# Kernel optimization log

Measured on AMD Instinct MI355X. Metric: run time of the kernel, lower is better.

The kernel has to match this reference:

```python
import jax, jax.numpy as jnp
import numpy as np

E = 32          # n_routed_experts
H = 2048        # hidden_size
I = 1024        # moe_intermediate_size
T = 32768       # total routed tokens (grouped/sorted by expert)


def setup_inputs() -> dict:
    key = jax.random.key(0)
    k1, k2, k3 = jax.random.split(key, 3)
    x = jax.random.normal(k1, (T, H), dtype=jnp.float32)
    # per-expert weights: fused w1/w3 -> [E, H, 2I], w2 -> [E, I, H]
    w13 = jax.random.normal(k2, (E, H, 2 * I), dtype=jnp.float32) * (1.0 / np.sqrt(H))
    w2 = jax.random.normal(k3, (E, I, H), dtype=jnp.float32) * (1.0 / np.sqrt(I))
    tokens_per_expert = jnp.full((E,), T // E, dtype=jnp.int32)  # uniform groups
    decoding = 0  # unused flag (prefill path)
    return {"x": x, "w13": w13, "w2": w2,
            "tokens_per_expert": tokens_per_expert, "decoding": decoding}


def reference(x, w13, w2, tokens_per_expert, decoding):
    # Grouped GEMM expert FFN with SwiGLU. Tokens are grouped (sorted) by
    # expert; with uniform tokens_per_expert the ragged grouped GEMM is the
    # block-diagonal einsum below (g = tokens per expert group).
    e = w13.shape[0]
    t = x.shape[0]
    g = t // e
    xg = x.reshape(e, g, x.shape[-1])            # [E, g, H]
    gate_up = jnp.einsum('egi,eio->ego', xg, w13)  # [E, g, 2I]
    gate, up = jnp.split(gate_up, 2, axis=-1)
    h = jax.nn.silu(gate) * up                    # fused SwiGLU epilogue
    out = jnp.einsum('egi,eio->ego', h, w2)       # [E, g, H]
    return out.reshape(t, -1)
```

## Files before the change

kernel.cpp:

```cpp
#include <hip/hip_runtime.h>
#include <hip/hip_bf16.h>

#define NE 32
#define HD 2048
#define ID 1024
#define GT 1024

#define BK 64

typedef __attribute__((ext_vector_type(8))) __bf16 bf16x8;
typedef __attribute__((ext_vector_type(4))) float  f32x4;

__device__ __forceinline__ __bf16 f2b(float f) { return (__bf16)f; }

__device__ __forceinline__ bf16x8 pack8(const f32x4 a, const f32x4 b) {
  bf16x8 v;
  v[0] = f2b(a[0]); v[1] = f2b(a[1]); v[2] = f2b(a[2]); v[3] = f2b(a[3]);
  v[4] = f2b(b[0]); v[5] = f2b(b[1]); v[6] = f2b(b[2]); v[7] = f2b(b[3]);
  return v;
}

__global__ __launch_bounds__(256)
void cvt_x_bf16(const float* __restrict__ x, __bf16* __restrict__ xb) {
  size_t i = ((size_t)blockIdx.x * 256 + threadIdx.x) * 8;
  f32x4 a = *reinterpret_cast<const f32x4*>(x + i);
  f32x4 b = *reinterpret_cast<const f32x4*>(x + i + 4);
  *reinterpret_cast<bf16x8*>(xb + i) = pack8(a, b);
}

__global__ __launch_bounds__(512, 2)
void moe_gemm1_swiglu_bA(const __bf16* __restrict__ xb,
                         const float* __restrict__ w13,
                         __bf16* __restrict__ h) {
  __shared__ __bf16 As[2][256][BK];
  __shared__ __bf16 Bg[2][128][BK];
  __shared__ __bf16 Bu[2][128][BK];

  const int t = threadIdx.x;
  const int bid  = blockIdx.x;
  const int work = (bid & 7) * 128 + (bid >> 3);
  const int e    = work >> 5;
  const int rem  = work & 31;
  const int n0   = (rem >> 2) * 128;
  const int m0   = (rem & 3) * 256;

  const __bf16* xA = xb + (size_t)(e * GT + m0) * HD;
  const float*  wB = w13 + (size_t)e * HD * (2 * ID);

  const int wid = t >> 6, lane = t & 63;
  const int wm = wid >> 2, wn = wid & 3;
  const int fr = lane & 15, fq = lane >> 4;

  const int tb = t & 255;
  const int nq = tb & 31;
  const int ko = tb >> 5;
  const int bcol = (t < 256 ? 0 : ID) + n0 + nq * 4;
  __bf16 (*Bm)[128][BK] = (t < 256) ? Bg : Bu;

  f32x4 accg[8][2];
  f32x4 accu[8][2];
#pragma unroll
  for (int i = 0; i < 8; ++i)
#pragma unroll
    for (int j = 0; j < 2; ++j) { accg[i][j] = 0.f; accu[i][j] = 0.f; }

  bf16x8 raa[4];
  f32x4 rb[8];

#define LOAD_TILE1(K0)                                                         \
  do {                                                                         \
    _Pragma("unroll")                                                          \
    for (int i = 0; i < 4; ++i) {                                              \
      int id = i * 512 + t;                                                    \
      int koA = id & 7, m = id >> 3;                                           \
      raa[i] = *reinterpret_cast<const bf16x8*>(xA + (size_t)m * HD + (K0) + koA * 8); \
    }                                                                          \
    const float* pb = wB + (size_t)((K0) + ko * 8) * (2 * ID) + bcol;          \
    _Pragma("unroll")                                                          \
    for (int j = 0; j < 8; ++j)                                                \
      rb[j] = *reinterpret_cast<const f32x4*>(pb + (size_t)j * (2 * ID));      \
  } while (0)

#define STORE_TILE1(P)                                                         \
  do {                                                                         \
    _Pragma("unroll")                                                          \
    for (int i = 0; i < 4; ++i) {                                              \
      int id = i * 512 + t;                                                    \
      int koA = id & 7, m = id >> 3;                                           \
      *reinterpret_cast<bf16x8*>(&As[P][m][(koA ^ (m & 7)) * 8]) = raa[i];     \
    }                                                                          \
    _Pragma("unroll")                                                          \
    for (int c = 0; c < 4; ++c) {                                              \
      int row = nq * 4 + c;                                                    \
      int slot = (ko ^ ((row >> 1) & 7)) * 8;                                  \
      bf16x8 v;                                                                \
      _Pragma("unroll")                                                        \
      for (int j = 0; j < 8; ++j) v[j] = f2b(rb[j][c]);                        \
      *reinterpret_cast<bf16x8*>(&Bm[P][row][slot]) = v;                       \
    }                                                                          \
  } while (0)

#define MFMA_HALF1(P, KB)                                                      \
  do {                                                                         \
    bf16x8 af[8], bgf[2], buf2[2];                                             \
    _Pragma("unroll")                                                          \
    for (int mi = 0; mi < 8; ++mi) {                                           \
      int row = wm * 128 + mi * 16 + fr;                                       \
      int oct = (fq + (KB)) ^ (row & 7);                                       \
      af[mi] = *reinterpret_cast<const bf16x8*>(&As[P][row][oct * 8]);         \
    }                                                                          \
    _Pragma("unroll")                                                          \
    for (int ni = 0; ni < 2; ++ni) {                                           \
      int row = wn * 32 + ni * 16 + fr;                                        \
      int oct = (fq + (KB)) ^ ((row >> 1) & 7);                                \
      bgf[ni]  = *reinterpret_cast<const bf16x8*>(&Bg[P][row][oct * 8]);       \
      buf2[ni] = *reinterpret_cast<const bf16x8*>(&Bu[P][row][oct * 8]);       \
    }                                                                          \
    __builtin_amdgcn_s_setprio(1);                                             \
    _Pragma("unroll")                                                          \
    for (int mi = 0; mi < 8; ++mi)                                             \
      _Pragma("unroll")                                                        \
      for (int ni = 0; ni < 2; ++ni) {                                         \
        accg[mi][ni] = __builtin_amdgcn_mfma_f32_16x16x32_bf16(                \
            af[mi], bgf[ni], accg[mi][ni], 0, 0, 0);                           \
        accu[mi][ni] = __builtin_amdgcn_mfma_f32_16x16x32_bf16(                \
            af[mi], buf2[ni], accu[mi][ni], 0, 0, 0);                          \
      }                                                                        \
    __builtin_amdgcn_s_setprio(0);                                             \
  } while (0)

  LOAD_TILE1(0);
  STORE_TILE1(0);
  LOAD_TILE1(BK);
  asm volatile("s_waitcnt lgkmcnt(0)" ::: "memory");
  __builtin_amdgcn_s_barrier();

  for (int k0 = 0, p = 0; k0 < HD; k0 += BK, p ^= 1) {
    MFMA_HALF1(p, 0);
    if (k0 + BK < HD) STORE_TILE1(p ^ 1);
    MFMA_HALF1(p, 4);
    if (k0 + 2 * BK < HD) LOAD_TILE1(k0 + 2 * BK);
    asm volatile("s_waitcnt lgkmcnt(0)" ::: "memory");
    __builtin_amdgcn_s_barrier();
  }
#undef LOAD_TILE1
#undef STORE_TILE1
#undef MFMA_HALF1

#pragma unroll
  for (int mi = 0; mi < 8; ++mi)
#pragma unroll
    for (int ni = 0; ni < 2; ++ni)
#pragma unroll
      for (int j = 0; j < 4; ++j) {
        int row = m0 + wm * 128 + mi * 16 + fq * 4 + j;
        int col = n0 + wn * 32 + ni * 16 + fr;
        float g = accg[mi][ni][j];
        float u = accu[mi][ni][j];
        float s = g / (1.f + __expf(-g));
        h[(size_t)(e * GT + row) * ID + col] = f2b(s * u);
      }
}

__global__ __launch_bounds__(256, 2)
void moe_gemm1_swiglu(const float* __restrict__ x,
                      const float* __restrict__ w13,
                      __bf16* __restrict__ h) {
  __shared__ __bf16 As[2][128][BK];
  __shared__ __bf16 Bg[2][64][BK];
  __shared__ __bf16 Bu[2][64][BK];

  const int t  = threadIdx.x;
  const int e  = blockIdx.z;
  const int m0 = blockIdx.y * 128;
  const int n0 = blockIdx.x * 64;

  const float* xA = x   + (size_t)(e * GT + m0) * HD;
  const float* wB = w13 + (size_t)e * HD * (2 * ID);

  const int wid = t >> 6, lane = t & 63;
  const int wm = wid >> 1, wn = wid & 1;
  const int fr = lane & 15, fq = lane >> 4;

  const int tb = t & 127;
  const int nq = tb & 15;
  const int ko = tb >> 4;
  const int bcol = (t < 128 ? 0 : ID) + n0 + nq * 4;
  __bf16 (*Bm)[64][BK] = (t < 128) ? Bg : Bu;

  f32x4 accg[4][2];
  f32x4 accu[4][2];
#pragma unroll
  for (int i = 0; i < 4; ++i)
#pragma unroll
    for (int j = 0; j < 2; ++j) { accg[i][j] = 0.f; accu[i][j] = 0.f; }

  f32x4 ra[4][2];
  f32x4 rb[8];

#define LOAD_TILE1(K0)                                                         \
  do {                                                                         \
    _Pragma("unroll")                                                          \
    for (int i = 0; i < 4; ++i) {                                              \
      int id = i * 256 + t;                                                    \
      int r = id >> 3, oc = id & 7;                                            \
      const float* src = xA + (size_t)r * HD + (K0) + oc * 8;                  \
      ra[i][0] = *reinterpret_cast<const f32x4*>(src);                         \
      ra[i][1] = *reinterpret_cast<const f32x4*>(src + 4);                     \
    }                                                                          \
    const float* pb = wB + (size_t)((K0) + ko * 8) * (2 * ID) + bcol;          \
    _Pragma("unroll")                                                          \
    for (int j = 0; j < 8; ++j)                                                \
      rb[j] = *reinterpret_cast<const f32x4*>(pb + (size_t)j * (2 * ID));      \
  } while (0)

#define STORE_TILE1(P)                                                         \
  do {                                                                         \
    _Pragma("unroll")                                                          \
    for (int i = 0; i < 4; ++i) {                                              \
      int id = i * 256 + t;                                                    \
      int r = id >> 3, oc = id & 7;                                            \
      *reinterpret_cast<bf16x8*>(&As[P][r][(oc ^ (r & 7)) * 8]) =              \
          pack8(ra[i][0], ra[i][1]);                                           \
    }                                                                          \
    _Pragma("unroll")                                                          \
    for (int c = 0; c < 4; ++c) {                                              \
      int row = nq * 4 + c;                                                    \
      int slot = (ko ^ ((row >> 1) & 7)) * 8;                                  \
      bf16x8 v;                                                                \
      _Pragma("unroll")                                                        \
      for (int j = 0; j < 8; ++j) v[j] = f2b(rb[j][c]);                        \
      *reinterpret_cast<bf16x8*>(&Bm[P][row][slot]) = v;                       \
    }                                                                          \
  } while (0)

#define MFMA_HALF1(P, KB)                                                      \
  do {                                                                         \
    bf16x8 af[4], bgf[2], buf2[2];                                             \
    _Pragma("unroll")                                                          \
    for (int mi = 0; mi < 4; ++mi) {                                           \
      int row = wm * 64 + mi * 16 + fr;                                        \
      int oct = (fq + (KB)) ^ (row & 7);                                       \
      af[mi] = *reinterpret_cast<const bf16x8*>(&As[P][row][oct * 8]);         \
    }                                                                          \
    _Pragma("unroll")                                                          \
    for (int ni = 0; ni < 2; ++ni) {                                           \
      int row = wn * 32 + ni * 16 + fr;                                        \
      int oct = (fq + (KB)) ^ ((row >> 1) & 7);                                \
      bgf[ni]  = *reinterpret_cast<const bf16x8*>(&Bg[P][row][oct * 8]);       \
      buf2[ni] = *reinterpret_cast<const bf16x8*>(&Bu[P][row][oct * 8]);       \
    }                                                                          \
    __builtin_amdgcn_s_setprio(1);                                             \
    _Pragma("unroll")                                                          \
    for (int mi = 0; mi < 4; ++mi)                                             \
      _Pragma("unroll")                                                        \
      for (int ni = 0; ni < 2; ++ni) {                                         \
        accg[mi][ni] = __builtin_amdgcn_mfma_f32_16x16x32_bf16(                \
            af[mi], bgf[ni], accg[mi][ni], 0, 0, 0);                           \
        accu[mi][ni] = __builtin_amdgcn_mfma_f32_16x16x32_bf16(                \
            af[mi], buf2[ni], accu[mi][ni], 0, 0, 0);                          \
      }                                                                        \
    __builtin_amdgcn_s_setprio(0);                                             \
  } while (0)

  LOAD_TILE1(0);
  STORE_TILE1(0);
  LOAD_TILE1(BK);
  asm volatile("s_waitcnt lgkmcnt(0)" ::: "memory");
  __builtin_amdgcn_s_barrier();

  for (int k0 = 0, p = 0; k0 < HD; k0 += BK, p ^= 1) {
    MFMA_HALF1(p, 0);
    if (k0 + BK < HD) STORE_TILE1(p ^ 1);
    MFMA_HALF1(p, 4);
    if (k0 + 2 * BK < HD) LOAD_TILE1(k0 + 2 * BK);
    asm volatile("s_waitcnt lgkmcnt(0)" ::: "memory");
    __builtin_amdgcn_s_barrier();
  }
#undef LOAD_TILE1
#undef STORE_TILE1
#undef MFMA_HALF1

#pragma unroll
  for (int mi = 0; mi < 4; ++mi)
#pragma unroll
    for (int ni = 0; ni < 2; ++ni)
#pragma unroll
      for (int j = 0; j < 4; ++j) {
        int row = m0 + wm * 64 + mi * 16 + fq * 4 + j;
        int col = n0 + wn * 32 + ni * 16 + fr;
        float g = accg[mi][ni][j];
        float u = accu[mi][ni][j];
        float s = g / (1.f + __expf(-g));
        h[(size_t)(e * GT + row) * ID + col] = f2b(s * u);
      }
}

__global__ __launch_bounds__(512, 2)
void moe_gemm2(const __bf16* __restrict__ h,
               const float* __restrict__ w2,
               float* __restrict__ out) {
  __shared__ __bf16 As[2][256][BK];
  __shared__ __bf16 Bs[2][256][BK];

  const int t = threadIdx.x;
  const int bid  = blockIdx.x;
  const int work = (bid & 7) * 128 + (bid >> 3);
  const int e    = work >> 5;
  const int rem  = work & 31;
  const int n0   = (rem >> 2) * 256;
  const int m0   = (rem & 3) * 256;

  const __bf16* hA = h  + (size_t)(e * GT + m0) * ID;
  const float*  wB = w2 + (size_t)e * ID * HD;

  const int wid = t >> 6, lane = t & 63;
  const int wm = wid >> 2, wn = wid & 3;
  const int fr = lane & 15, fq = lane >> 4;

  const int nq = t & 63;
  const int ko = t >> 6;

  f32x4 acc[8][4];
#pragma unroll
  for (int i = 0; i < 8; ++i)
#pragma unroll
    for (int j = 0; j < 4; ++j) acc[i][j] = 0.f;

  bf16x8 raa[4];
  f32x4 rb[8];

#define LOAD_TILE2(K0)                                                         \
  do {                                                                         \
    _Pragma("unroll")                                                          \
    for (int i = 0; i < 4; ++i) {                                              \
      int id = i * 512 + t;                                                    \
      int koA = id & 7, m = id >> 3;                                           \
      raa[i] = *reinterpret_cast<const bf16x8*>(hA + (size_t)m * ID + (K0) + koA * 8); \
    }                                                                          \
    const float* pg = wB + (size_t)((K0) + ko * 8) * HD + (n0 + nq * 4);       \
    _Pragma("unroll")                                                          \
    for (int j = 0; j < 8; ++j)                                                \
      rb[j] = *reinterpret_cast<const f32x4*>(pg + (size_t)j * HD);            \
  } while (0)

#define STORE_TILE2(P)                                                         \
  do {                                                                         \
    _Pragma("unroll")                                                          \
    for (int i = 0; i < 4; ++i) {                                              \
      int id = i * 512 + t;                                                    \
      int koA = id & 7, m = id >> 3;                                           \
      *reinterpret_cast<bf16x8*>(&As[P][m][(koA ^ (m & 7)) * 8]) = raa[i];     \
    }                                                                          \
    _Pragma("unroll")                                                          \
    for (int c = 0; c < 4; ++c) {                                              \
      int row = nq * 4 + c;                                                    \
      int slot = (ko ^ ((row >> 1) & 7)) * 8;                                  \
      bf16x8 v;                                                                \
      _Pragma("unroll")                                                        \
      for (int j = 0; j < 8; ++j) v[j] = f2b(rb[j][c]);                        \
      *reinterpret_cast<bf16x8*>(&Bs[P][row][slot]) = v;                       \
    }                                                                          \
  } while (0)

#define MFMA_HALF2(P, KB)                                                      \
  do {                                                                         \
    bf16x8 af[8], bf[4];                                                       \
    _Pragma("unroll")                                                          \
    for (int mi = 0; mi < 8; ++mi) {                                           \
      int row = wm * 128 + mi * 16 + fr;                                       \
      int oct = (fq + (KB)) ^ (row & 7);                                       \
      af[mi] = *reinterpret_cast<const bf16x8*>(&As[P][row][oct * 8]);         \
    }                                                                          \
    _Pragma("unroll")                                                          \
    for (int ni = 0; ni < 4; ++ni) {                                           \
      int row = wn * 64 + ni * 16 + fr;                                        \
      int oct = (fq + (KB)) ^ ((row >> 1) & 7);                                \
      bf[ni] = *reinterpret_cast<const bf16x8*>(&Bs[P][row][oct * 8]);         \
    }                                                                          \
    __builtin_amdgcn_s_setprio(1);                                             \
    _Pragma("unroll")                                                          \
    for (int mi = 0; mi < 8; ++mi)                                             \
      _Pragma("unroll")                                                        \
      for (int ni = 0; ni < 4; ++ni)                                           \
        acc[mi][ni] = __builtin_amdgcn_mfma_f32_16x16x32_bf16(                 \
            af[mi], bf[ni], acc[mi][ni], 0, 0, 0);                             \
    __builtin_amdgcn_s_setprio(0);                                             \
  } while (0)

  LOAD_TILE2(0);
  STORE_TILE2(0);
  LOAD_TILE2(BK);
  asm volatile("s_waitcnt lgkmcnt(0)" ::: "memory");
  __builtin_amdgcn_s_barrier();

  for (int k0 = 0, p = 0; k0 < ID; k0 += BK, p ^= 1) {
    MFMA_HALF2(p, 0);
    if (k0 + BK < ID) STORE_TILE2(p ^ 1);
    MFMA_HALF2(p, 4);
    if (k0 + 2 * BK < ID) LOAD_TILE2(k0 + 2 * BK);
    asm volatile("s_waitcnt lgkmcnt(0)" ::: "memory");
    __builtin_amdgcn_s_barrier();
  }
#undef LOAD_TILE2
#undef STORE_TILE2
#undef MFMA_HALF2

#pragma unroll
  for (int mi = 0; mi < 8; ++mi)
#pragma unroll
    for (int ni = 0; ni < 4; ++ni)
#pragma unroll
      for (int j = 0; j < 4; ++j) {
        int row = m0 + wm * 128 + mi * 16 + fq * 4 + j;
        int col = n0 + wn * 64 + ni * 16 + fr;
        out[(size_t)(e * GT + row) * HD + col] = acc[mi][ni][j];
      }
}

extern "C" void kernel_launch(void* const* d_in, const int* in_sizes, int n_in,
                              void* d_out, int out_size, void* d_ws, size_t ws_size,
                              hipStream_t stream) {
  const float* x   = (const float*)d_in[0];
  const float* w13 = (const float*)d_in[1];
  const float* w2  = (const float*)d_in[2];
  float* out = (float*)d_out;

  const size_t H_BYTES  = (size_t)GT * NE * ID * sizeof(__bf16);
  const size_t XB_BYTES = (size_t)GT * NE * HD * sizeof(__bf16);
  __bf16* h  = (__bf16*)d_ws;
  __bf16* xb = (__bf16*)((char*)d_ws + H_BYTES);

  if (ws_size >= H_BYTES + XB_BYTES) {
    cvt_x_bf16<<<dim3((GT * NE * (HD / 8)) / 256), dim3(256), 0, stream>>>(x, xb);
    moe_gemm1_swiglu_bA<<<dim3(1024), dim3(512), 0, stream>>>(xb, w13, h);
  } else {
    moe_gemm1_swiglu<<<dim3(ID / 64, GT / 128, NE), dim3(256), 0, stream>>>(x, w13, h);
  }
  moe_gemm2<<<dim3(1024), dim3(512), 0, stream>>>(h, w2, out);
}
```

Before: 560.1 us.

## Interleave global loads, LDS stores and MFMA in four barrier-separated phases

Both GEMM main loops are rewritten into a four-phase schedule, ping-pong style. Each phase reads a subset of fragments from LDS and does one part of the staging work: storing A, prefetching A, storing B, or prefetching B. Each phase then runs a block of MFMAs between workgroup barriers. The aim is to spread memory traffic across the MFMA work so waves overlap compute with loads instead of bunching all stores and loads at two points. The extra barriers per iteration add synchronisation cost, and keeping the A fragments live across phases raises register pressure.

```diff
diff --git a/kernel.cpp b/kernel.cpp
--- a/kernel.cpp
+++ b/kernel.cpp
@@ -19,6 +19,9 @@
   v[4] = f2b(b[0]); v[5] = f2b(b[1]); v[6] = f2b(b[2]); v[7] = f2b(b[3]);
   return v;
 }
+
+#define SBAR() __builtin_amdgcn_s_barrier()
+#define LGKM0() asm volatile("s_waitcnt lgkmcnt(0)" ::: "memory")
 
 __global__ __launch_bounds__(256)
 void cvt_x_bf16(const float* __restrict__ x, __bf16* __restrict__ xb) {
@@ -67,7 +70,7 @@
   bf16x8 raa[4];
   f32x4 rb[8];
 
-#define LOAD_TILE1(K0)                                                         \
+#define LOAD_A1(K0)                                                            \
   do {                                                                         \
     _Pragma("unroll")                                                          \
     for (int i = 0; i < 4; ++i) {                                              \
@@ -75,13 +78,17 @@
       int koA = id & 7, m = id >> 3;                                           \
       raa[i] = *reinterpret_cast<const bf16x8*>(xA + (size_t)m * HD + (K0) + koA * 8); \
     }                                                                          \
+  } while (0)
+
+#define LOAD_B1(K0)                                                            \
+  do {                                                                         \
     const float* pb = wB + (size_t)((K0) + ko * 8) * (2 * ID) + bcol;          \
     _Pragma("unroll")                                                          \
     for (int j = 0; j < 8; ++j)                                                \
       rb[j] = *reinterpret_cast<const f32x4*>(pb + (size_t)j * (2 * ID));      \
   } while (0)
 
-#define STORE_TILE1(P)                                                         \
+#define STORE_A1(P)                                                            \
   do {                                                                         \
     _Pragma("unroll")                                                          \
     for (int i = 0; i < 4; ++i) {                                              \
@@ -89,6 +96,10 @@
       int koA = id & 7, m = id >> 3;                                           \
       *reinterpret_cast<bf16x8*>(&As[P][m][(koA ^ (m & 7)) * 8]) = raa[i];     \
     }                                                                          \
+  } while (0)
+
+#define STORE_B1(P)                                                            \
+  do {                                                                         \
     _Pragma("unroll")                                                          \
     for (int c = 0; c < 4; ++c) {                                              \
       int row = nq * 4 + c;                                                    \
@@ -100,52 +111,98 @@
     }                                                                          \
   } while (0)
 
-#define MFMA_HALF1(P, KB)                                                      \
-  do {                                                                         \
-    bf16x8 af[8], bgf[2], buf2[2];                                             \
-    _Pragma("unroll")                                                          \
-    for (int mi = 0; mi < 8; ++mi) {                                           \
-      int row = wm * 128 + mi * 16 + fr;                                       \
-      int oct = (fq + (KB)) ^ (row & 7);                                       \
-      af[mi] = *reinterpret_cast<const bf16x8*>(&As[P][row][oct * 8]);         \
-    }                                                                          \
-    _Pragma("unroll")                                                          \
-    for (int ni = 0; ni < 2; ++ni) {                                           \
-      int row = wn * 32 + ni * 16 + fr;                                        \
-      int oct = (fq + (KB)) ^ ((row >> 1) & 7);                                \
-      bgf[ni]  = *reinterpret_cast<const bf16x8*>(&Bg[P][row][oct * 8]);       \
-      buf2[ni] = *reinterpret_cast<const bf16x8*>(&Bu[P][row][oct * 8]);       \
-    }                                                                          \
-    __builtin_amdgcn_s_setprio(1);                                             \
-    _Pragma("unroll")                                                          \
-    for (int mi = 0; mi < 8; ++mi)                                             \
-      _Pragma("unroll")                                                        \
-      for (int ni = 0; ni < 2; ++ni) {                                         \
-        accg[mi][ni] = __builtin_amdgcn_mfma_f32_16x16x32_bf16(                \
-            af[mi], bgf[ni], accg[mi][ni], 0, 0, 0);                           \
-        accu[mi][ni] = __builtin_amdgcn_mfma_f32_16x16x32_bf16(                \
-            af[mi], buf2[ni], accu[mi][ni], 0, 0, 0);                          \
-      }                                                                        \
-    __builtin_amdgcn_s_setprio(0);                                             \
-  } while (0)
-
-  LOAD_TILE1(0);
-  STORE_TILE1(0);
-  LOAD_TILE1(BK);
-  asm volatile("s_waitcnt lgkmcnt(0)" ::: "memory");
-  __builtin_amdgcn_s_barrier();
+  LOAD_A1(0);
+  LOAD_B1(0);
+  STORE_A1(0);
+  STORE_B1(0);
+  LOAD_A1(BK);
+  LOAD_B1(BK);
+  LGKM0();
+  SBAR();
 
   for (int k0 = 0, p = 0; k0 < HD; k0 += BK, p ^= 1) {
-    MFMA_HALF1(p, 0);
-    if (k0 + BK < HD) STORE_TILE1(p ^ 1);
-    MFMA_HALF1(p, 4);
-    if (k0 + 2 * BK < HD) LOAD_TILE1(k0 + 2 * BK);
-    asm volatile("s_waitcnt lgkmcnt(0)" ::: "memory");
-    __builtin_amdgcn_s_barrier();
+    const bool stg = (k0 + BK < HD);
+    const bool pre = (k0 + 2 * BK < HD);
+    bf16x8 af[8], bgf[2], buv[2];
+
+#pragma unroll
+    for (int mi = 0; mi < 8; ++mi) {
+      int row = wm * 128 + mi * 16 + fr;
+      af[mi] = *reinterpret_cast<const bf16x8*>(&As[p][row][(fq ^ (row & 7)) * 8]);
+    }
+#pragma unroll
+    for (int ni = 0; ni < 2; ++ni) {
+      int row = wn * 32 + ni * 16 + fr;
+      bgf[ni] = *reinterpret_cast<const bf16x8*>(&Bg[p][row][(fq ^ ((row >> 1) & 7)) * 8]);
+    }
+    SBAR(); LGKM0();
+    __builtin_amdgcn_s_setprio(1);
+#pragma unroll
+    for (int mi = 0; mi < 8; ++mi)
+#pragma unroll
+      for (int ni = 0; ni < 2; ++ni)
+        accg[mi][ni] = __builtin_amdgcn_mfma_f32_16x16x32_bf16(af[mi], bgf[ni], accg[mi][ni], 0, 0, 0);
+    __builtin_amdgcn_s_setprio(0);
+    SBAR();
+
+#pragma unroll
+    for (int ni = 0; ni < 2; ++ni) {
+      int row = wn * 32 + ni * 16 + fr;
+      buv[ni] = *reinterpret_cast<const bf16x8*>(&Bu[p][row][(fq ^ ((row >> 1) & 7)) * 8]);
+    }
+    if (stg) STORE_A1(p ^ 1);
+    if (pre) LOAD_A1(k0 + 2 * BK);
+    SBAR(); LGKM0();
+    __builtin_amdgcn_s_setprio(1);
+#pragma unroll
+    for (int mi = 0; mi < 8; ++mi)
+#pragma unroll
+      for (int ni = 0; ni < 2; ++ni)
+        accu[mi][ni] = __builtin_amdgcn_mfma_f32_16x16x32_bf16(af[mi], buv[ni], accu[mi][ni], 0, 0, 0);
+    __builtin_amdgcn_s_setprio(0);
+    SBAR();
+
+#pragma unroll
+    for (int mi = 0; mi < 8; ++mi) {
+      int row = wm * 128 + mi * 16 + fr;
+      af[mi] = *reinterpret_cast<const bf16x8*>(&As[p][row][((fq + 4) ^ (row & 7)) * 8]);
+    }
+#pragma unroll
+    for (int ni = 0; ni < 2; ++ni) {
+      int row = wn * 32 + ni * 16 + fr;
+      bgf[ni] = *reinterpret_cast<const bf16x8*>(&Bg[p][row][((fq + 4) ^ ((row >> 1) & 7)) * 8]);
+    }
+    if (stg) STORE_B1(p ^ 1);
+    SBAR(); LGKM0();
+    __builtin_amdgcn_s_setprio(1);
+#pragma unroll
+    for (int mi = 0; mi < 8; ++mi)
+#pragma unroll
+      for (int ni = 0; ni < 2; ++ni)
+        accg[mi][ni] = __builtin_amdgcn_mfma_f32_16x16x32_bf16(af[mi], bgf[ni], accg[mi][ni], 0, 0, 0);
+    __builtin_amdgcn_s_setprio(0);
+    SBAR();
+
+#pragma unroll
+    for (int ni = 0; ni < 2; ++ni) {
+      int row = wn * 32 + ni * 16 + fr;
+      buv[ni] = *reinterpret_cast<const bf16x8*>(&Bu[p][row][((fq + 4) ^ ((row >> 1) & 7)) * 8]);
+    }
+    if (pre) LOAD_B1(k0 + 2 * BK);
+    SBAR(); LGKM0();
+    __builtin_amdgcn_s_setprio(1);
+#pragma unroll
+    for (int mi = 0; mi < 8; ++mi)
+#pragma unroll
+      for (int ni = 0; ni < 2; ++ni)
+        accu[mi][ni] = __builtin_amdgcn_mfma_f32_16x16x32_bf16(af[mi], buv[ni], accu[mi][ni], 0, 0, 0);
+    __builtin_amdgcn_s_setprio(0);
+    SBAR();
   }
-#undef LOAD_TILE1
-#undef STORE_TILE1
-#undef MFMA_HALF1
+#undef LOAD_A1
+#undef LOAD_B1
+#undef STORE_A1
+#undef STORE_B1
 
 #pragma unroll
   for (int mi = 0; mi < 8; ++mi)
@@ -266,16 +323,16 @@
   LOAD_TILE1(0);
   STORE_TILE1(0);
   LOAD_TILE1(BK);
-  asm volatile("s_waitcnt lgkmcnt(0)" ::: "memory");
-  __builtin_amdgcn_s_barrier();
+  LGKM0();
+  SBAR();
 
   for (int k0 = 0, p = 0; k0 < HD; k0 += BK, p ^= 1) {
     MFMA_HALF1(p, 0);
     if (k0 + BK < HD) STORE_TILE1(p ^ 1);
     MFMA_HALF1(p, 4);
     if (k0 + 2 * BK < HD) LOAD_TILE1(k0 + 2 * BK);
-    asm volatile("s_waitcnt lgkmcnt(0)" ::: "memory");
-    __builtin_amdgcn_s_barrier();
+    LGKM0();
+    SBAR();
   }
 #undef LOAD_TILE1
 #undef STORE_TILE1
@@ -330,7 +387,7 @@
   bf16x8 raa[4];
   f32x4 rb[8];
 
-#define LOAD_TILE2(K0)                                                         \
+#define LOAD_A2(K0)                                                            \
   do {                                                                         \
     _Pragma("unroll")                                                          \
     for (int i = 0; i < 4; ++i) {                                              \
@@ -338,13 +395,17 @@
       int koA = id & 7, m = id >> 3;                                           \
       raa[i] = *reinterpret_cast<const bf16x8*>(hA + (size_t)m * ID + (K0) + koA * 8); \
     }                                                                          \
+  } while (0)
+
+#define LOAD_B2(K0)                                                            \
+  do {                                                                         \
     const float* pg = wB + (size_t)((K0) + ko * 8) * HD + (n0 + nq * 4);       \
     _Pragma("unroll")                                                          \
     for (int j = 0; j < 8; ++j)                                                \
       rb[j] = *reinterpret_cast<const f32x4*>(pg + (size_t)j * HD);            \
   } while (0)
 
-#define STORE_TILE2(P)                                                         \
+#define STORE_A2(P)                                                            \
   do {                                                                         \
     _Pragma("unroll")                                                          \
     for (int i = 0; i < 4; ++i) {                                              \
@@ -352,6 +413,10 @@
       int koA = id & 7, m = id >> 3;                                           \
       *reinterpret_cast<bf16x8*>(&As[P][m][(koA ^ (m & 7)) * 8]) = raa[i];     \
     }                                                                          \
+  } while (0)
+
+#define STORE_B2(P)                                                            \
+  do {                                                                         \
     _Pragma("unroll")                                                          \
     for (int c = 0; c < 4; ++c) {                                              \
       int row = nq * 4 + c;                                                    \
@@ -363,48 +428,98 @@
     }                                                                          \
   } while (0)
 
-#define MFMA_HALF2(P, KB)                                                      \
-  do {                                                                         \
-    bf16x8 af[8], bf[4];                                                       \
-    _Pragma("unroll")                                                          \
-    for (int mi = 0; mi < 8; ++mi) {                                           \
-      int row = wm * 128 + mi * 16 + fr;                                       \
-      int oct = (fq + (KB)) ^ (row & 7);                                       \
-      af[mi] = *reinterpret_cast<const bf16x8*>(&As[P][row][oct * 8]);         \
-    }                                                                          \
-    _Pragma("unroll")                                                          \
-    for (int ni = 0; ni < 4; ++ni) {                                           \
-      int row = wn * 64 + ni * 16 + fr;                                        \
-      int oct = (fq + (KB)) ^ ((row >> 1) & 7);                                \
-      bf[ni] = *reinterpret_cast<const bf16x8*>(&Bs[P][row][oct * 8]);         \
-    }                                                                          \
-    __builtin_amdgcn_s_setprio(1);                                             \
-    _Pragma("unroll")                                                          \
-    for (int mi = 0; mi < 8; ++mi)                                             \
-      _Pragma("unroll")                                                        \
-      for (int ni = 0; ni < 4; ++ni)                                           \
-        acc[mi][ni] = __builtin_amdgcn_mfma_f32_16x16x32_bf16(                 \
-            af[mi], bf[ni], acc[mi][ni], 0, 0, 0);                             \
-    __builtin_amdgcn_s_setprio(0);                                             \
-  } while (0)
-
-  LOAD_TILE2(0);
-  STORE_TILE2(0);
-  LOAD_TILE2(BK);
-  asm volatile("s_waitcnt lgkmcnt(0)" ::: "memory");
-  __builtin_amdgcn_s_barrier();
+  LOAD_A2(0);
+  LOAD_B2(0);
+  STORE_A2(0);
+  STORE_B2(0);
+  LOAD_A2(BK);
+  LOAD_B2(BK);
+  LGKM0();
+  SBAR();
 
   for (int k0 = 0, p = 0; k0 < ID; k0 += BK, p ^= 1) {
-    MFMA_HALF2(p, 0);
-    if (k0 + BK < ID) STORE_TILE2(p ^ 1);
-    MFMA_HALF2(p, 4);
-    if (k0 + 2 * BK < ID) LOAD_TILE2(k0 + 2 * BK);
-    asm volatile("s_waitcnt lgkmcnt(0)" ::: "memory");
-    __builtin_amdgcn_s_barrier();
+    const bool stg = (k0 + BK < ID);
+    const bool pre = (k0 + 2 * BK < ID);
+    bf16x8 af[8], bf[2];
+
+#pragma unroll
+    for (int mi = 0; mi < 8; ++mi) {
+      int row = wm * 128 + mi * 16 + fr;
+      af[mi] = *reinterpret_cast<const bf16x8*>(&As[p][row][(fq ^ (row & 7)) * 8]);
+    }
+#pragma unroll
+    for (int ni = 0; ni < 2; ++ni) {
+      int row = wn * 64 + ni * 16 + fr;
+      bf[ni] = *reinterpret_cast<const bf16x8*>(&Bs[p][row][(fq ^ ((row >> 1) & 7)) * 8]);
+    }
+    SBAR(); LGKM0();
+    __builtin_amdgcn_s_setprio(1);
+#pragma unroll
+    for (int mi = 0; mi < 8; ++mi)
+#pragma unroll
+      for (int ni = 0; ni < 2; ++ni)
+        acc[mi][ni] = __builtin_amdgcn_mfma_f32_16x16x32_bf16(af[mi], bf[ni], acc[mi][ni], 0, 0, 0);
+    __builtin_amdgcn_s_setprio(0);
+    SBAR();
+
+#pragma unroll
+    for (int ni = 0; ni < 2; ++ni) {
+      int row = wn * 64 + (ni + 2) * 16 + fr;
+      bf[ni] = *reinterpret_cast<const bf16x8*>(&Bs[p][row][(fq ^ ((row >> 1) & 7)) * 8]);
+    }
+    if (stg) STORE_A2(p ^ 1);
+    if (pre) LOAD_A2(k0 + 2 * BK);
+    SBAR(); LGKM0();
+    __builtin_amdgcn_s_setprio(1);
+#pragma unroll
+    for (int mi = 0; mi < 8; ++mi)
+#pragma unroll
+      for (int ni = 0; ni < 2; ++ni)
+        acc[mi][ni + 2] = __builtin_amdgcn_mfma_f32_16x16x32_bf16(af[mi], bf[ni], acc[mi][ni + 2], 0, 0, 0);
+    __builtin_amdgcn_s_setprio(0);
+    SBAR();
+
+#pragma unroll
+    for (int mi = 0; mi < 8; ++mi) {
+      int row = wm * 128 + mi * 16 + fr;
+      af[mi] = *reinterpret_cast<const bf16x8*>(&As[p][row][((fq + 4) ^ (row & 7)) * 8]);
+    }
+#pragma unroll
+    for (int ni = 0; ni < 2; ++ni) {
+      int row = wn * 64 + ni * 16 + fr;
+      bf[ni] = *reinterpret_cast<const bf16x8*>(&Bs[p][row][((fq + 4) ^ ((row >> 1) & 7)) * 8]);
+    }
+    if (stg) STORE_B2(p ^ 1);
+    SBAR(); LGKM0();
+    __builtin_amdgcn_s_setprio(1);
+#pragma unroll
+    for (int mi = 0; mi < 8; ++mi)
+#pragma unroll
+      for (int ni = 0; ni < 2; ++ni)
+        acc[mi][ni] = __builtin_amdgcn_mfma_f32_16x16x32_bf16(af[mi], bf[ni], acc[mi][ni], 0, 0, 0);
+    __builtin_amdgcn_s_setprio(0);
+    SBAR();
+
+#pragma unroll
+    for (int ni = 0; ni < 2; ++ni) {
+      int row = wn * 64 + (ni + 2) * 16 + fr;
+      bf[ni] = *reinterpret_cast<const bf16x8*>(&Bs[p][row][((fq + 4) ^ ((row >> 1) & 7)) * 8]);
+    }
+    if (pre) LOAD_B2(k0 + 2 * BK);
+    SBAR(); LGKM0();
+    __builtin_amdgcn_s_setprio(1);
+#pragma unroll
+    for (int mi = 0; mi < 8; ++mi)
+#pragma unroll
+      for (int ni = 0; ni < 2; ++ni)
+        acc[mi][ni + 2] = __builtin_amdgcn_mfma_f32_16x16x32_bf16(af[mi], bf[ni], acc[mi][ni + 2], 0, 0, 0);
+    __builtin_amdgcn_s_setprio(0);
+    SBAR();
   }
-#undef LOAD_TILE2
-#undef STORE_TILE2
-#undef MFMA_HALF2
+#undef LOAD_A2
+#undef LOAD_B2
+#undef STORE_A2
+#undef STORE_B2
 
 #pragma unroll
   for (int mi = 0; mi < 8; ++mi)
```

After: 645.3 us. 15.2% more time.
